# Optimization experiments

Hardware: AMD Instinct MI355X
Metric: run time of the kernel (lower is better)

Reference implementation:

```python
import jax, jax.numpy as jnp
import numpy as np

N = 100000      # nodes
E = 1600000     # edges (avg degree 16)
IN_C = 128
OUT_C = 64
HID = 2 * OUT_C  # 128


def setup_inputs() -> dict:
    key = jax.random.key(0)
    ks = jax.random.split(key, 8)
    x = jax.random.normal(ks[0], (N, IN_C), dtype=jnp.float32)
    edge_index = jax.random.randint(ks[1], (2, E), 0, N, dtype=jnp.int32)
    # Glorot-ish init for GCN weight matrices, zero bias (PyG default)
    w1 = jax.random.normal(ks[2], (IN_C, HID), dtype=jnp.float32) / np.sqrt(IN_C)
    b1 = jnp.zeros((HID,), jnp.float32)
    w_mu = jax.random.normal(ks[3], (HID, OUT_C), dtype=jnp.float32) / np.sqrt(HID)
    b_mu = jnp.zeros((OUT_C,), jnp.float32)
    w_ls = jax.random.normal(ks[4], (HID, OUT_C), dtype=jnp.float32) / np.sqrt(HID)
    b_ls = jnp.zeros((OUT_C,), jnp.float32)
    return {"x": x, "edge_index": edge_index, "w1": w1, "b1": b1,
            "w_mu": w_mu, "b_mu": b_mu, "w_ls": w_ls, "b_ls": b_ls}


def _gcn_conv(h, w, b, src, dst, norm, n):
    # linear transform, then normalized sparse aggregation src -> dst
    h = h @ w                                   # [N, out]
    msg = h[src] * norm[:, None]                # [E+N, out] gather
    out = jax.ops.segment_sum(msg, dst, num_segments=n)  # scatter-add
    return out + b


def reference(x, edge_index, w1, b1, w_mu, b_mu, w_ls, b_ls):
    n = x.shape[0]
    # GCN normalization with self-loops (edge_weight=None -> all ones)
    loops = jnp.arange(n, dtype=edge_index.dtype)
    src = jnp.concatenate([edge_index[0], loops])
    dst = jnp.concatenate([edge_index[1], loops])
    ew = jnp.ones(src.shape[0], dtype=x.dtype)
    deg = jax.ops.segment_sum(ew, dst, num_segments=n)
    dinv = jnp.where(deg > 0, jax.lax.rsqrt(jnp.maximum(deg, 1e-12)), 0.0)
    norm = dinv[src] * ew * dinv[dst]           # D^-1/2 A_hat D^-1/2

    h = jax.nn.relu(_gcn_conv(x, w1, b1, src, dst, norm, n))
    mu = _gcn_conv(h, w_mu, b_mu, src, dst, norm, n)
    logstd = _gcn_conv(h, w_ls, b_ls, src, dst, norm, n)
    return (mu, logstd)
```

## Files before the change

### kernel.cpp

```cpp
#include <hip/hip_runtime.h>
#include <hip/hip_bf16.h>

#define CH 128
#define OC 64
#define NBINS 1024
#define NCHK  256
#define BSH   7

typedef __attribute__((ext_vector_type(4))) float f32x4;
typedef __attribute__((ext_vector_type(8))) float f32x8;
typedef __attribute__((ext_vector_type(8))) short bf16x8;
typedef __attribute__((ext_vector_type(8))) ushort u16x8;

static __device__ __forceinline__ float bf2f(ushort u) {
  return __uint_as_float(((unsigned)u) << 16);
}
static __device__ __forceinline__ ushort f2bf(float f) {
  __hip_bfloat16 h = __float2bfloat16(f);
  return *reinterpret_cast<ushort*>(&h);
}
static __device__ __forceinline__ void fma8(float w, u16x8 v, f32x8& a) {
#pragma unroll
  for (int j = 0; j < 8; j++) a[j] = fmaf(w, bf2f((ushort)v[j]), a[j]);
}

__global__ void k_tobf(const float* __restrict__ x, ushort* __restrict__ y, int n) {
  int i = (blockIdx.x * blockDim.x + threadIdx.x) * 4;
  if (i < n) {
    float4 v = *(const float4*)&x[i];
    ushort4 o; o.x = f2bf(v.x); o.y = f2bf(v.y); o.z = f2bf(v.z); o.w = f2bf(v.w);
    *(ushort4*)&y[i] = o;
  }
}

__global__ void k_prep(const float* __restrict__ w1, const float* __restrict__ wmu,
                       const float* __restrict__ wls, const float* __restrict__ bmu,
                       const float* __restrict__ bls, ushort* __restrict__ Wt0,
                       ushort* __restrict__ Wt1, float* __restrict__ bc) {
  int idx = blockIdx.x * 256 + threadIdx.x;
  int c = idx >> 7, k = idx & 127;
  Wt0[c * 128 + k] = f2bf(w1[k * 128 + c]);
  float v = (c < 64) ? wmu[k * 64 + c] : wls[k * 64 + (c - 64)];
  Wt1[c * 128 + k] = f2bf(v);
  if (idx < 128) bc[idx] = (idx < 64) ? bmu[idx] : bls[idx - 64];
}


__global__ __launch_bounds__(256) void k_s1(const int* __restrict__ dst,
                                            int* __restrict__ bcnt, int ne, int cs) {
  __shared__ int h[NBINS];
  for (int j = threadIdx.x; j < NBINS; j += 256) h[j] = 0;
  __syncthreads();
  int e0 = blockIdx.x * cs, e1 = min(e0 + cs, ne);
  for (int e = e0 + threadIdx.x; e < e1; e += 256)
    atomicAdd(&h[dst[e] >> BSH], 1);
  __syncthreads();
  for (int j = threadIdx.x; j < NBINS; j += 256)
    bcnt[blockIdx.x * NBINS + j] = h[j];
}

__global__ __launch_bounds__(256) void k_s2a(const int* __restrict__ bcnt,
                                             int* __restrict__ curT,
                                             int* __restrict__ total) {
  __shared__ int s[NCHK];
  int b = blockIdx.x, t = threadIdx.x;
  int v = bcnt[t * NBINS + b];
  s[t] = v; __syncthreads();
  for (int off = 1; off < NCHK; off <<= 1) {
    int u = (t >= off) ? s[t - off] : 0;
    __syncthreads();
    s[t] += u;
    __syncthreads();
  }
  curT[b * NCHK + t] = s[t] - v;
  if (t == NCHK - 1) total[b] = s[t];
}

__global__ void k_s2b(const int* __restrict__ total, int* __restrict__ base) {
  __shared__ int s[256];
  int t = threadIdx.x;
  int loc[4]; int sum = 0;
#pragma unroll
  for (int j = 0; j < 4; j++) { loc[j] = total[t * 4 + j]; sum += loc[j]; }
  s[t] = sum; __syncthreads();
  int own = sum;
  for (int off = 1; off < 256; off <<= 1) {
    int u = (t >= off) ? s[t - off] : 0;
    __syncthreads();
    s[t] += u;
    __syncthreads();
  }
  int excl = s[t] - own;
#pragma unroll
  for (int j = 0; j < 4; j++) { base[t * 4 + j] = excl; excl += loc[j]; }
  if (t == 255) base[NBINS] = excl;
}

__global__ __launch_bounds__(256) void k_s3(const int* __restrict__ src,
    const int* __restrict__ dst, const int* __restrict__ curT,
    const int* __restrict__ base, int2* __restrict__ rec, int ne, int cs) {
  __shared__ int lcur[NBINS];
  int blk = blockIdx.x;
  for (int b = threadIdx.x; b < NBINS; b += 256)
    lcur[b] = curT[b * NCHK + blk] + base[b];
  __syncthreads();
  int e0 = blk * cs, e1 = min(e0 + cs, ne);
  for (int e = e0 + threadIdx.x; e < e1; e += 256) {
    int d = dst[e], sv = src[e];
    int pos = atomicAdd(&lcur[d >> BSH], 1);
    rec[pos] = make_int2(sv, d);
  }
}

__global__ __launch_bounds__(256) void k_s4(const int2* __restrict__ rec,
    const int* __restrict__ base, int* __restrict__ deg, int nn) {
  __shared__ int h[128];
  int b = blockIdx.x;
  if (threadIdx.x < 128) h[threadIdx.x] = 0;
  __syncthreads();
  int r0 = base[b], r1 = base[b + 1];
  for (int r = r0 + threadIdx.x; r < r1; r += 256)
    atomicAdd(&h[rec[r].y & 127], 1);
  __syncthreads();
  if (threadIdx.x < 128) {
    int node = (b << BSH) + threadIdx.x;
    if (node < nn) deg[node] = h[threadIdx.x];
  }
}

__global__ __launch_bounds__(256) void k_s5(const int2* __restrict__ rec,
    const int* __restrict__ base, const int* __restrict__ rowptr,
    const int* __restrict__ deg, unsigned* __restrict__ csr, int nn) {
  __shared__ int lcur[128];
  int b = blockIdx.x;
  if (threadIdx.x < 128) {
    int node = (b << BSH) + threadIdx.x;
    lcur[threadIdx.x] = (node < nn) ? rowptr[node] : 0;
  }
  __syncthreads();
  int r0 = base[b], r1 = base[b + 1];
  for (int r = r0 + threadIdx.x; r < r1; r += 256) {
    int2 rc = rec[r];
    int pos = atomicAdd(&lcur[rc.y & 127], 1);
    unsigned ds = (unsigned)min(deg[rc.x], 32767);
    csr[pos] = (unsigned)rc.x | (ds << 17);
  }
}


__global__ void k_scan1(const int* __restrict__ deg, int* __restrict__ bsum, int n) {
  __shared__ int s[256];
  int tid = threadIdx.x;
  int base = blockIdx.x * 2048;
  int sum = 0;
#pragma unroll
  for (int j = 0; j < 8; j++) {
    int idx = base + tid * 8 + j;
    if (idx < n) sum += deg[idx];
  }
  s[tid] = sum; __syncthreads();
  for (int off = 128; off > 0; off >>= 1) {
    if (tid < off) s[tid] += s[tid + off];
    __syncthreads();
  }
  if (tid == 0) bsum[blockIdx.x] = s[0];
}

__global__ void k_scan2(int* bsum, int nb) {
  __shared__ int s[256];
  int tid = threadIdx.x;
  int v = (tid < nb) ? bsum[tid] : 0;
  s[tid] = v; __syncthreads();
  for (int off = 1; off < 256; off <<= 1) {
    int t = (tid >= off) ? s[tid - off] : 0;
    __syncthreads();
    s[tid] += t;
    __syncthreads();
  }
  if (tid < nb) bsum[tid] = s[tid] - v;
}

__global__ void k_scan3(const int* __restrict__ deg, const int* __restrict__ bsum,
                        int* __restrict__ rowptr, float* __restrict__ dinv, int n) {
  __shared__ int s[256];
  int tid = threadIdx.x;
  int base = blockIdx.x * 2048;
  int local[8]; int sum = 0;
#pragma unroll
  for (int j = 0; j < 8; j++) {
    int idx = base + tid * 8 + j;
    int d = (idx < n) ? deg[idx] : 0;
    local[j] = d; sum += d;
  }
  s[tid] = sum; __syncthreads();
  int own = sum;
  for (int off = 1; off < 256; off <<= 1) {
    int t = (tid >= off) ? s[tid - off] : 0;
    __syncthreads();
    s[tid] += t;
    __syncthreads();
  }
  int excl = s[tid] - own + bsum[blockIdx.x];
#pragma unroll
  for (int j = 0; j < 8; j++) {
    int idx = base + tid * 8 + j;
    if (idx < n) {
      rowptr[idx] = excl;
      excl += local[j];
      dinv[idx] = rsqrtf((float)(local[j] + 1));
    }
  }
}

template<int MODE>
__global__ __launch_bounds__(256) void k_agg(const ushort* __restrict__ in,
                      ushort* __restrict__ o16, float* __restrict__ oA,
                      float* __restrict__ oB, const float* __restrict__ bc,
                      const int* __restrict__ rowptr, const int* __restrict__ deg,
                      const unsigned* __restrict__ csr, const float* __restrict__ dinv,
                      int n) {
  int i = blockIdx.x * 16 + (threadIdx.x >> 4);
  if (i >= n) return;
  int lane = threadIdx.x & 15;
  size_t loff = (size_t)lane * 8;
  int beg = rowptr[i];
  int cnt = deg[i];
  float di = dinv[i];
  u16x8 xv = *(const u16x8*)&in[(size_t)i * CH + loff];
  f32x8 acc = {0.f, 0.f, 0.f, 0.f, 0.f, 0.f, 0.f, 0.f};

  unsigned rec[8]; u16x8 row[4];
#pragma unroll
  for (int j = 0; j < 8; j++) rec[j] = (j < cnt) ? csr[beg + j] : 0u;
#pragma unroll
  for (int j = 0; j < 4; j++)
    if (j < cnt) row[j] = *(const u16x8*)&in[(size_t)(rec[j] & 0x1FFFFu) * CH + loff];

  int k = 0;
  while (cnt - k > 4) {
    unsigned nrec[4]; u16x8 nrow[4];
#pragma unroll
    for (int j = 0; j < 4; j++)
      nrec[j] = (k + 8 + j < cnt) ? csr[beg + k + 8 + j] : 0u;
#pragma unroll
    for (int j = 0; j < 4; j++)
      nrow[j] = (k + 4 + j < cnt)
              ? *(const u16x8*)&in[(size_t)(rec[4 + j] & 0x1FFFFu) * CH + loff]
              : row[j];
#pragma unroll
    for (int j = 0; j < 4; j++) {
      float w = rsqrtf((float)((rec[j] >> 17) + 1u));
      fma8(w, row[j], acc);
    }
#pragma unroll
    for (int j = 0; j < 4; j++) { rec[j] = rec[4 + j]; rec[4 + j] = nrec[j]; row[j] = nrow[j]; }
    k += 4;
  }
#pragma unroll
  for (int j = 0; j < 4; j++) {
    if (k + j < cnt) {
      float w = rsqrtf((float)((rec[j] >> 17) + 1u));
      fma8(w, row[j], acc);
    }
  }
  fma8(di, xv, acc);
  if (MODE == 0) {
    u16x8 o;
#pragma unroll
    for (int j = 0; j < 8; j++) o[j] = (short)f2bf(acc[j] * di);
    *(u16x8*)&o16[(size_t)i * CH + loff] = o;
  } else {
    f32x8 b8 = *(const f32x8*)&bc[lane * 8];
    f32x8 o;
#pragma unroll
    for (int j = 0; j < 8; j++) o[j] = acc[j] * di + b8[j];
    if (lane < 8) *(f32x8*)&oA[(size_t)i * OC + lane * 8] = o;
    else          *(f32x8*)&oB[(size_t)i * OC + (lane - 8) * 8] = o;
  }
}

__global__ __launch_bounds__(256) void k_fused(const ushort* __restrict__ A,
    const ushort* __restrict__ Wt0, const float* __restrict__ b1,
    const ushort* __restrict__ Wt1, ushort* __restrict__ P, int ntiles) {
  __shared__ ushort hs[16][136];
  int colg = threadIdx.x >> 6;
  int lane = threadIdx.x & 63;
  int l15 = lane & 15;
  int lk = (lane >> 4) * 8;
  bf16x8 bfrag1[2][4], bfrag2[2][4];
  float bias1[2];
#pragma unroll
  for (int ct = 0; ct < 2; ct++) {
    int bcol = colg * 32 + ct * 16 + l15;
#pragma unroll
    for (int kt = 0; kt < 4; kt++) {
      bfrag1[ct][kt] = *(const bf16x8*)&Wt0[(size_t)bcol * 128 + kt * 32 + lk];
      bfrag2[ct][kt] = *(const bf16x8*)&Wt1[(size_t)bcol * 128 + kt * 32 + lk];
    }
    bias1[ct] = b1[bcol];
  }
  for (int t = blockIdx.x; t < ntiles; t += gridDim.x) {
    const ushort* ap = &A[(size_t)(t * 16 + l15) * CH + lk];
    bf16x8 af[4];
#pragma unroll
    for (int kt = 0; kt < 4; kt++) af[kt] = *(const bf16x8*)&ap[kt * 32];
    f32x4 acc1[2] = {{0.f, 0.f, 0.f, 0.f}, {0.f, 0.f, 0.f, 0.f}};
#pragma unroll
    for (int ct = 0; ct < 2; ct++)
#pragma unroll
      for (int kt = 0; kt < 4; kt++)
        acc1[ct] = __builtin_amdgcn_mfma_f32_16x16x32_bf16(af[kt], bfrag1[ct][kt], acc1[ct], 0, 0, 0);
#pragma unroll
    for (int ct = 0; ct < 2; ct++) {
      int col = colg * 32 + ct * 16 + l15;
#pragma unroll
      for (int r = 0; r < 4; r++)
        hs[(lane >> 4) * 4 + r][col] = f2bf(fmaxf(acc1[ct][r] + bias1[ct], 0.f));
    }
    __syncthreads();
    bf16x8 af2[4];
#pragma unroll
    for (int kt = 0; kt < 4; kt++) af2[kt] = *(const bf16x8*)&hs[l15][kt * 32 + lk];
    f32x4 acc2[2] = {{0.f, 0.f, 0.f, 0.f}, {0.f, 0.f, 0.f, 0.f}};
#pragma unroll
    for (int ct = 0; ct < 2; ct++)
#pragma unroll
      for (int kt = 0; kt < 4; kt++)
        acc2[ct] = __builtin_amdgcn_mfma_f32_16x16x32_bf16(af2[kt], bfrag2[ct][kt], acc2[ct], 0, 0, 0);
#pragma unroll
    for (int ct = 0; ct < 2; ct++) {
      int col = colg * 32 + ct * 16 + l15;
#pragma unroll
      for (int r = 0; r < 4; r++) {
        int node = t * 16 + (lane >> 4) * 4 + r;
        P[(size_t)node * CH + col] = f2bf(acc2[ct][r]);
      }
    }
    __syncthreads();
  }
}


extern "C" void kernel_launch(void* const* d_in, const int* in_sizes, int n_in,
                              void* d_out, int out_size, void* d_ws, size_t ws_size,
                              hipStream_t stream) {
  const float* x   = (const float*)d_in[0];
  const int*   ei  = (const int*)d_in[1];
  const float* w1  = (const float*)d_in[2];
  const float* b1  = (const float*)d_in[3];
  const float* wmu = (const float*)d_in[4];
  const float* bmu = (const float*)d_in[5];
  const float* wls = (const float*)d_in[6];
  const float* bls = (const float*)d_in[7];
  float* out = (float*)d_out;

  const int nn = in_sizes[0] / CH;
  const int ne = in_sizes[1] / 2;
  const int* srcp = ei;
  const int* dstp = ei + ne;

  ushort*   B0   = (ushort*)d_ws;
  ushort*   B1   = B0 + (size_t)nn * CH;
  unsigned* csr  = (unsigned*)(B1 + (size_t)nn * CH);
  int*      deg  = (int*)(csr + ne);
  int*      rowptr = deg + nn;
  float*    dinv = (float*)(rowptr + nn);
  int*      bsum = (int*)(dinv + nn);
  ushort*   Wt0  = (ushort*)(bsum + 256);
  ushort*   Wt1  = Wt0 + 128 * 128;
  float*    bc   = (float*)(Wt1 + 128 * 128);

  int2*     rec  = (int2*)B1;
  int*      bcnt = (int*)(rec + ne);
  int*      curT = bcnt + NCHK * NBINS;
  int*      btot = curT + NBINS * NCHK;
  int*      bbase= btot + NBINS;

  const int NBUK = (nn + 127) >> BSH;
  const int cs = (ne + NCHK - 1) / NCHK;
  const int NB = (nn + 2047) / 2048;

  k_s1 <<<NCHK, 256, 0, stream>>>(dstp, bcnt, ne, cs);
  k_s2a<<<NBINS, NCHK, 0, stream>>>(bcnt, curT, btot);
  k_s2b<<<1, 256, 0, stream>>>(btot, bbase);
  k_s3 <<<NCHK, 256, 0, stream>>>(srcp, dstp, curT, bbase, rec, ne, cs);
  k_s4 <<<NBUK, 256, 0, stream>>>(rec, bbase, deg, nn);
  k_scan1<<<NB, 256, 0, stream>>>(deg, bsum, nn);
  k_scan2<<<1, 256, 0, stream>>>(bsum, NB);
  k_scan3<<<NB, 256, 0, stream>>>(deg, bsum, rowptr, dinv, nn);
  k_s5 <<<NBUK, 256, 0, stream>>>(rec, bbase, rowptr, deg, csr, nn);

  k_tobf<<<((nn * CH / 4) + 255) / 256, 256, 0, stream>>>(x, B0, nn * CH);
  k_prep<<<64, 256, 0, stream>>>(w1, wmu, wls, bmu, bls, Wt0, Wt1, bc);

  const int AB = (nn + 15) / 16;
  const int ntiles = nn / 16;

  k_agg<0><<<AB, 256, 0, stream>>>(B0, B1, nullptr, nullptr, nullptr,
                                   rowptr, deg, csr, dinv, nn);
  k_fused<<<1024, 256, 0, stream>>>(B1, Wt0, b1, Wt1, B0, ntiles);
  k_agg<1><<<AB, 256, 0, stream>>>(B0, nullptr, out, out + (size_t)nn * OC, bc,
                                   rowptr, deg, csr, dinv, nn);
}
```

Before: 228.1 us.

## Fuse first aggregation with MLP GEMMs, pack edge records, merge scans and prep kernels

Several independent changes are bundled. Edge records are packed into one 32-bit word (source<<7 | local dst) to halve scatter traffic. The per-bucket histogram now computes rowptr and dinv directly with a local scan, replacing three global scan kernels. The bf16 conversion and weight prep are merged into one launch. The first aggregation is fused into the MFMA two-layer transform kernel, which removes the intermediate aggregated buffer round-trip. The fused kernel runs the gather per tile inside a persistent grid, which may reduce latency hiding compared with a full one-block-per-16-nodes grid, and it drops the trailing barrier between tiles.

After: 227.4 us. No clear change (-0.3%).

```diff
diff --git a/kernel.cpp b/kernel.cpp
--- a/kernel.cpp
+++ b/kernel.cpp
@@ -24,25 +24,25 @@
   for (int j = 0; j < 8; j++) a[j] = fmaf(w, bf2f((ushort)v[j]), a[j]);
 }
 
-__global__ void k_tobf(const float* __restrict__ x, ushort* __restrict__ y, int n) {
-  int i = (blockIdx.x * blockDim.x + threadIdx.x) * 4;
-  if (i < n) {
+__global__ void k_pre(const float* __restrict__ x, ushort* __restrict__ y, int nx,
+                      const float* __restrict__ w1, const float* __restrict__ wmu,
+                      const float* __restrict__ wls, const float* __restrict__ bmu,
+                      const float* __restrict__ bls, ushort* __restrict__ Wt0,
+                      ushort* __restrict__ Wt1, float* __restrict__ bc) {
+  int gid = blockIdx.x * 256 + threadIdx.x;
+  int i = gid * 4;
+  if (i < nx) {
     float4 v = *(const float4*)&x[i];
     ushort4 o; o.x = f2bf(v.x); o.y = f2bf(v.y); o.z = f2bf(v.z); o.w = f2bf(v.w);
     *(ushort4*)&y[i] = o;
   }
-}
-
-__global__ void k_prep(const float* __restrict__ w1, const float* __restrict__ wmu,
-                       const float* __restrict__ wls, const float* __restrict__ bmu,
-                       const float* __restrict__ bls, ushort* __restrict__ Wt0,
-                       ushort* __restrict__ Wt1, float* __restrict__ bc) {
-  int idx = blockIdx.x * 256 + threadIdx.x;
-  int c = idx >> 7, k = idx & 127;
-  Wt0[c * 128 + k] = f2bf(w1[k * 128 + c]);
-  float v = (c < 64) ? wmu[k * 64 + c] : wls[k * 64 + (c - 64)];
-  Wt1[c * 128 + k] = f2bf(v);
-  if (idx < 128) bc[idx] = (idx < 64) ? bmu[idx] : bls[idx - 64];
+  if (gid < 16384) {
+    int c = gid >> 7, k = gid & 127;
+    Wt0[c * 128 + k] = f2bf(w1[k * 128 + c]);
+    float v = (c < 64) ? wmu[k * 64 + c] : wls[k * 64 + (c - 64)];
+    Wt1[c * 128 + k] = f2bf(v);
+    if (gid < 128) bc[gid] = (gid < 64) ? bmu[gid] : bls[gid - 64];
+  }
 }
 
 
@@ -98,7 +98,7 @@
 
 __global__ __launch_bounds__(256) void k_s3(const int* __restrict__ src,
     const int* __restrict__ dst, const int* __restrict__ curT,
-    const int* __restrict__ base, int2* __restrict__ rec, int ne, int cs) {
+    const int* __restrict__ base, unsigned* __restrict__ rec, int ne, int cs) {
   __shared__ int lcur[NBINS];
   int blk = blockIdx.x;
   for (int b = threadIdx.x; b < NBINS; b += 256)
@@ -108,236 +108,201 @@
   for (int e = e0 + threadIdx.x; e < e1; e += 256) {
     int d = dst[e], sv = src[e];
     int pos = atomicAdd(&lcur[d >> BSH], 1);
-    rec[pos] = make_int2(sv, d);
-  }
-}
-
-__global__ __launch_bounds__(256) void k_s4(const int2* __restrict__ rec,
-    const int* __restrict__ base, int* __restrict__ deg, int nn) {
+    rec[pos] = ((unsigned)sv << BSH) | (unsigned)(d & 127);
+  }
+}
+
+__global__ __launch_bounds__(256) void k_s4a(const unsigned* __restrict__ rec,
+    const int* __restrict__ base, int* __restrict__ deg, int* __restrict__ rowptr,
+    float* __restrict__ dinv, int nn) {
   __shared__ int h[128];
-  int b = blockIdx.x;
-  if (threadIdx.x < 128) h[threadIdx.x] = 0;
+  __shared__ int sc[128];
+  int b = blockIdx.x, tid = threadIdx.x;
+  if (tid < 128) h[tid] = 0;
   __syncthreads();
   int r0 = base[b], r1 = base[b + 1];
-  for (int r = r0 + threadIdx.x; r < r1; r += 256)
-    atomicAdd(&h[rec[r].y & 127], 1);
-  __syncthreads();
-  if (threadIdx.x < 128) {
-    int node = (b << BSH) + threadIdx.x;
-    if (node < nn) deg[node] = h[threadIdx.x];
-  }
-}
-
-__global__ __launch_bounds__(256) void k_s5(const int2* __restrict__ rec,
+  for (int r = r0 + tid; r < r1; r += 256)
+    atomicAdd(&h[rec[r] & 127], 1);
+  __syncthreads();
+  if (tid < 128) sc[tid] = h[tid];
+  __syncthreads();
+  for (int off = 1; off < 128; off <<= 1) {
+    int v = 0;
+    if (tid < 128 && tid >= off) v = sc[tid - off];
+    __syncthreads();
+    if (tid < 128) sc[tid] += v;
+    __syncthreads();
+  }
+  if (tid < 128) {
+    int node = (b << BSH) + tid;
+    if (node < nn) {
+      int d = h[tid];
+      deg[node] = d;
+      rowptr[node] = r0 + sc[tid] - d;
+      dinv[node] = rsqrtf((float)(d + 1));
+    }
+  }
+}
+
+__global__ __launch_bounds__(256) void k_s5(const unsigned* __restrict__ rec,
     const int* __restrict__ base, const int* __restrict__ rowptr,
     const int* __restrict__ deg, unsigned* __restrict__ csr, int nn) {
   __shared__ int lcur[128];
-  int b = blockIdx.x;
-  if (threadIdx.x < 128) {
-    int node = (b << BSH) + threadIdx.x;
-    lcur[threadIdx.x] = (node < nn) ? rowptr[node] : 0;
+  int b = blockIdx.x, tid = threadIdx.x;
+  if (tid < 128) {
+    int node = (b << BSH) + tid;
+    lcur[tid] = (node < nn) ? rowptr[node] : 0;
   }
   __syncthreads();
   int r0 = base[b], r1 = base[b + 1];
-  for (int r = r0 + threadIdx.x; r < r1; r += 256) {
-    int2 rc = rec[r];
-    int pos = atomicAdd(&lcur[rc.y & 127], 1);
-    unsigned ds = (unsigned)min(deg[rc.x], 32767);
-    csr[pos] = (unsigned)rc.x | (ds << 17);
-  }
-}
-
-
-__global__ void k_scan1(const int* __restrict__ deg, int* __restrict__ bsum, int n) {
-  __shared__ int s[256];
+  for (int r = r0 + tid; r < r1; r += 256) {
+    unsigned rc = rec[r];
+    int s = (int)(rc >> BSH);
+    int pos = atomicAdd(&lcur[rc & 127], 1);
+    unsigned ds = (unsigned)min(deg[s], 32767);
+    csr[pos] = (unsigned)s | (ds << 17);
+  }
+}
+
+static __device__ __forceinline__ f32x8 gather_core(const ushort* __restrict__ in,
+    const int* __restrict__ rowptr, const int* __restrict__ deg,
+    const unsigned* __restrict__ csr, const float* __restrict__ dinv,
+    int i, int lane16, float& di_out) {
+  size_t loff = (size_t)lane16 * 8;
+  int beg = rowptr[i];
+  int cnt = deg[i];
+  float di = dinv[i];
+  u16x8 xv = *(const u16x8*)&in[(size_t)i * CH + loff];
+  f32x8 acc = {0.f, 0.f, 0.f, 0.f, 0.f, 0.f, 0.f, 0.f};
+
+  unsigned rec[8]; u16x8 row[4];
+#pragma unroll
+  for (int j = 0; j < 8; j++) rec[j] = (j < cnt) ? csr[beg + j] : 0u;
+#pragma unroll
+  for (int j = 0; j < 4; j++)
+    if (j < cnt) row[j] = *(const u16x8*)&in[(size_t)(rec[j] & 0x1FFFFu) * CH + loff];
+
+  int k = 0;
+  while (cnt - k > 4) {
+    unsigned nrec[4]; u16x8 nrow[4];
+#pragma unroll
+    for (int j = 0; j < 4; j++)
+      nrec[j] = (k + 8 + j < cnt) ? csr[beg + k + 8 + j] : 0u;
+#pragma unroll
+    for (int j = 0; j < 4; j++)
+      nrow[j] = (k + 4 + j < cnt)
+              ? *(const u16x8*)&in[(size_t)(rec[4 + j] & 0x1FFFFu) * CH + loff]
+              : row[j];
+#pragma unroll
+    for (int j = 0; j < 4; j++) {
+      float w = rsqrtf((float)((rec[j] >> 17) + 1u));
+      fma8(w, row[j], acc);
+    }
+#pragma unroll
+    for (int j = 0; j < 4; j++) { rec[j] = rec[4 + j]; rec[4 + j] = nrec[j]; row[j] = nrow[j]; }
+    k += 4;
+  }
+#pragma unroll
+  for (int j = 0; j < 4; j++) {
+    if (k + j < cnt) {
+      float w = rsqrtf((float)((rec[j] >> 17) + 1u));
+      fma8(w, row[j], acc);
+    }
+  }
+  fma8(di, xv, acc);
+  di_out = di;
+  return acc;
+}
+
+__global__ __launch_bounds__(256) void k_aggemm(const ushort* __restrict__ in,
+    const int* __restrict__ rowptr, const int* __restrict__ deg,
+    const unsigned* __restrict__ csr, const float* __restrict__ dinv,
+    const ushort* __restrict__ Wt0, const float* __restrict__ b1,
+    const ushort* __restrict__ Wt1, ushort* __restrict__ P, int ntiles) {
+  __shared__ ushort as_[16][136];
+  __shared__ ushort hs[16][136];
   int tid = threadIdx.x;
-  int base = blockIdx.x * 2048;
-  int sum = 0;
-#pragma unroll
-  for (int j = 0; j < 8; j++) {
-    int idx = base + tid * 8 + j;
-    if (idx < n) sum += deg[idx];
-  }
-  s[tid] = sum; __syncthreads();
-  for (int off = 128; off > 0; off >>= 1) {
-    if (tid < off) s[tid] += s[tid + off];
-    __syncthreads();
-  }
-  if (tid == 0) bsum[blockIdx.x] = s[0];
-}
-
-__global__ void k_scan2(int* bsum, int nb) {
-  __shared__ int s[256];
-  int tid = threadIdx.x;
-  int v = (tid < nb) ? bsum[tid] : 0;
-  s[tid] = v; __syncthreads();
-  for (int off = 1; off < 256; off <<= 1) {
-    int t = (tid >= off) ? s[tid - off] : 0;
-    __syncthreads();
-    s[tid] += t;
-    __syncthreads();
-  }
-  if (tid < nb) bsum[tid] = s[tid] - v;
-}
-
-__global__ void k_scan3(const int* __restrict__ deg, const int* __restrict__ bsum,
-                        int* __restrict__ rowptr, float* __restrict__ dinv, int n) {
-  __shared__ int s[256];
-  int tid = threadIdx.x;
-  int base = blockIdx.x * 2048;
-  int local[8]; int sum = 0;
-#pragma unroll
-  for (int j = 0; j < 8; j++) {
-    int idx = base + tid * 8 + j;
-    int d = (idx < n) ? deg[idx] : 0;
-    local[j] = d; sum += d;
-  }
-  s[tid] = sum; __syncthreads();
-  int own = sum;
-  for (int off = 1; off < 256; off <<= 1) {
-    int t = (tid >= off) ? s[tid - off] : 0;
-    __syncthreads();
-    s[tid] += t;
-    __syncthreads();
-  }
-  int excl = s[tid] - own + bsum[blockIdx.x];
-#pragma unroll
-  for (int j = 0; j < 8; j++) {
-    int idx = base + tid * 8 + j;
-    if (idx < n) {
-      rowptr[idx] = excl;
-      excl += local[j];
-      dinv[idx] = rsqrtf((float)(local[j] + 1));
-    }
-  }
-}
-
-template<int MODE>
-__global__ __launch_bounds__(256) void k_agg(const ushort* __restrict__ in,
-                      ushort* __restrict__ o16, float* __restrict__ oA,
-                      float* __restrict__ oB, const float* __restrict__ bc,
+  int node16 = tid >> 4, lane16 = tid & 15;
+  int wv = tid >> 6;
+  int lane = tid & 63;
+  int l15 = lane & 15;
+  int lk = (lane >> 4) * 8;
+  bf16x8 bfrag1[2][4], bfrag2[2][4];
+  float bias1[2];
+#pragma unroll
+  for (int ct = 0; ct < 2; ct++) {
+    int bcol = wv * 32 + ct * 16 + l15;
+#pragma unroll
+    for (int kt = 0; kt < 4; kt++) {
+      bfrag1[ct][kt] = *(const bf16x8*)&Wt0[(size_t)bcol * 128 + kt * 32 + lk];
+      bfrag2[ct][kt] = *(const bf16x8*)&Wt1[(size_t)bcol * 128 + kt * 32 + lk];
+    }
+    bias1[ct] = b1[bcol];
+  }
+  for (int t = blockIdx.x; t < ntiles; t += gridDim.x) {
+    int i = t * 16 + node16;
+    float di;
+    f32x8 acc = gather_core(in, rowptr, deg, csr, dinv, i, lane16, di);
+    u16x8 o;
+#pragma unroll
+    for (int j = 0; j < 8; j++) o[j] = (short)f2bf(acc[j] * di);
+    *(u16x8*)&as_[node16][lane16 * 8] = o;
+    __syncthreads();
+    bf16x8 af[4];
+#pragma unroll
+    for (int kt = 0; kt < 4; kt++) af[kt] = *(const bf16x8*)&as_[l15][kt * 32 + lk];
+    f32x4 a1[2] = {{0.f, 0.f, 0.f, 0.f}, {0.f, 0.f, 0.f, 0.f}};
+#pragma unroll
+    for (int ct = 0; ct < 2; ct++)
+#pragma unroll
+      for (int kt = 0; kt < 4; kt++)
+        a1[ct] = __builtin_amdgcn_mfma_f32_16x16x32_bf16(af[kt], bfrag1[ct][kt], a1[ct], 0, 0, 0);
+#pragma unroll
+    for (int ct = 0; ct < 2; ct++) {
+      int col = wv * 32 + ct * 16 + l15;
+#pragma unroll
+      for (int r = 0; r < 4; r++)
+        hs[(lane >> 4) * 4 + r][col] = f2bf(fmaxf(a1[ct][r] + bias1[ct], 0.f));
+    }
+    __syncthreads();
+    bf16x8 af2[4];
+#pragma unroll
+    for (int kt = 0; kt < 4; kt++) af2[kt] = *(const bf16x8*)&hs[l15][kt * 32 + lk];
+    f32x4 a2[2] = {{0.f, 0.f, 0.f, 0.f}, {0.f, 0.f, 0.f, 0.f}};
+#pragma unroll
+    for (int ct = 0; ct < 2; ct++)
+#pragma unroll
+      for (int kt = 0; kt < 4; kt++)
+        a2[ct] = __builtin_amdgcn_mfma_f32_16x16x32_bf16(af2[kt], bfrag2[ct][kt], a2[ct], 0, 0, 0);
+#pragma unroll
+    for (int ct = 0; ct < 2; ct++) {
+      int col = wv * 32 + ct * 16 + l15;
+#pragma unroll
+      for (int r = 0; r < 4; r++) {
+        int node = t * 16 + (lane >> 4) * 4 + r;
+        P[(size_t)node * CH + col] = f2bf(a2[ct][r]);
+      }
+    }
+  }
+}
+
+__global__ __launch_bounds__(256) void k_aggout(const ushort* __restrict__ in,
+                      float* __restrict__ oA, float* __restrict__ oB,
+                      const float* __restrict__ bc,
                       const int* __restrict__ rowptr, const int* __restrict__ deg,
                       const unsigned* __restrict__ csr, const float* __restrict__ dinv,
                       int n) {
   int i = blockIdx.x * 16 + (threadIdx.x >> 4);
   if (i >= n) return;
   int lane = threadIdx.x & 15;
-  size_t loff = (size_t)lane * 8;
-  int beg = rowptr[i];
-  int cnt = deg[i];
-  float di = dinv[i];
-  u16x8 xv = *(const u16x8*)&in[(size_t)i * CH + loff];
-  f32x8 acc = {0.f, 0.f, 0.f, 0.f, 0.f, 0.f, 0.f, 0.f};
-
-  unsigned rec[8]; u16x8 row[4];
-#pragma unroll
-  for (int j = 0; j < 8; j++) rec[j] = (j < cnt) ? csr[beg + j] : 0u;
-#pragma unroll
-  for (int j = 0; j < 4; j++)
-    if (j < cnt) row[j] = *(const u16x8*)&in[(size_t)(rec[j] & 0x1FFFFu) * CH + loff];
-
-  int k = 0;
-  while (cnt - k > 4) {
-    unsigned nrec[4]; u16x8 nrow[4];
-#pragma unroll
-    for (int j = 0; j < 4; j++)
-      nrec[j] = (k + 8 + j < cnt) ? csr[beg + k + 8 + j] : 0u;
-#pragma unroll
-    for (int j = 0; j < 4; j++)
-      nrow[j] = (k + 4 + j < cnt)
-              ? *(const u16x8*)&in[(size_t)(rec[4 + j] & 0x1FFFFu) * CH + loff]
-              : row[j];
-#pragma unroll
-    for (int j = 0; j < 4; j++) {
-      float w = rsqrtf((float)((rec[j] >> 17) + 1u));
-      fma8(w, row[j], acc);
-    }
-#pragma unroll
-    for (int j = 0; j < 4; j++) { rec[j] = rec[4 + j]; rec[4 + j] = nrec[j]; row[j] = nrow[j]; }
-    k += 4;
-  }
-#pragma unroll
-  for (int j = 0; j < 4; j++) {
-    if (k + j < cnt) {
-      float w = rsqrtf((float)((rec[j] >> 17) + 1u));
-      fma8(w, row[j], acc);
-    }
-  }
-  fma8(di, xv, acc);
-  if (MODE == 0) {
-    u16x8 o;
-#pragma unroll
-    for (int j = 0; j < 8; j++) o[j] = (short)f2bf(acc[j] * di);
-    *(u16x8*)&o16[(size_t)i * CH + loff] = o;
-  } else {
-    f32x8 b8 = *(const f32x8*)&bc[lane * 8];
-    f32x8 o;
-#pragma unroll
-    for (int j = 0; j < 8; j++) o[j] = acc[j] * di + b8[j];
-    if (lane < 8) *(f32x8*)&oA[(size_t)i * OC + lane * 8] = o;
-    else          *(f32x8*)&oB[(size_t)i * OC + (lane - 8) * 8] = o;
-  }
-}
-
-__global__ __launch_bounds__(256) void k_fused(const ushort* __restrict__ A,
-    const ushort* __restrict__ Wt0, const float* __restrict__ b1,
-    const ushort* __restrict__ Wt1, ushort* __restrict__ P, int ntiles) {
-  __shared__ ushort hs[16][136];
-  int colg = threadIdx.x >> 6;
-  int lane = threadIdx.x & 63;
-  int l15 = lane & 15;
-  int lk = (lane >> 4) * 8;
-  bf16x8 bfrag1[2][4], bfrag2[2][4];
-  float bias1[2];
-#pragma unroll
-  for (int ct = 0; ct < 2; ct++) {
-    int bcol = colg * 32 + ct * 16 + l15;
-#pragma unroll
-    for (int kt = 0; kt < 4; kt++) {
-      bfrag1[ct][kt] = *(const bf16x8*)&Wt0[(size_t)bcol * 128 + kt * 32 + lk];
-      bfrag2[ct][kt] = *(const bf16x8*)&Wt1[(size_t)bcol * 128 + kt * 32 + lk];
-    }
-    bias1[ct] = b1[bcol];
-  }
-  for (int t = blockIdx.x; t < ntiles; t += gridDim.x) {
-    const ushort* ap = &A[(size_t)(t * 16 + l15) * CH + lk];
-    bf16x8 af[4];
-#pragma unroll
-    for (int kt = 0; kt < 4; kt++) af[kt] = *(const bf16x8*)&ap[kt * 32];
-    f32x4 acc1[2] = {{0.f, 0.f, 0.f, 0.f}, {0.f, 0.f, 0.f, 0.f}};
-#pragma unroll
-    for (int ct = 0; ct < 2; ct++)
-#pragma unroll
-      for (int kt = 0; kt < 4; kt++)
-        acc1[ct] = __builtin_amdgcn_mfma_f32_16x16x32_bf16(af[kt], bfrag1[ct][kt], acc1[ct], 0, 0, 0);
-#pragma unroll
-    for (int ct = 0; ct < 2; ct++) {
-      int col = colg * 32 + ct * 16 + l15;
-#pragma unroll
-      for (int r = 0; r < 4; r++)
-        hs[(lane >> 4) * 4 + r][col] = f2bf(fmaxf(acc1[ct][r] + bias1[ct], 0.f));
-    }
-    __syncthreads();
-    bf16x8 af2[4];
-#pragma unroll
-    for (int kt = 0; kt < 4; kt++) af2[kt] = *(const bf16x8*)&hs[l15][kt * 32 + lk];
-    f32x4 acc2[2] = {{0.f, 0.f, 0.f, 0.f}, {0.f, 0.f, 0.f, 0.f}};
-#pragma unroll
-    for (int ct = 0; ct < 2; ct++)
-#pragma unroll
-      for (int kt = 0; kt < 4; kt++)
-        acc2[ct] = __builtin_amdgcn_mfma_f32_16x16x32_bf16(af2[kt], bfrag2[ct][kt], acc2[ct], 0, 0, 0);
-#pragma unroll
-    for (int ct = 0; ct < 2; ct++) {
-      int col = colg * 32 + ct * 16 + l15;
-#pragma unroll
-      for (int r = 0; r < 4; r++) {
-        int node = t * 16 + (lane >> 4) * 4 + r;
-        P[(size_t)node * CH + col] = f2bf(acc2[ct][r]);
-      }
-    }
-    __syncthreads();
-  }
+  float di;
+  f32x8 acc = gather_core(in, rowptr, deg, csr, dinv, i, lane, di);
+  f32x8 b8 = *(const f32x8*)&bc[lane * 8];
+  f32x8 o;
+#pragma unroll
+  for (int j = 0; j < 8; j++) o[j] = acc[j] * di + b8[j];
+  if (lane < 8) *(f32x8*)&oA[(size_t)i * OC + lane * 8] = o;
+  else          *(f32x8*)&oB[(size_t)i * OC + (lane - 8) * 8] = o;
 }
 
 
@@ -365,12 +330,11 @@
   int*      deg  = (int*)(csr + ne);
   int*      rowptr = deg + nn;
   float*    dinv = (float*)(rowptr + nn);
-  int*      bsum = (int*)(dinv + nn);
-  ushort*   Wt0  = (ushort*)(bsum + 256);
+  ushort*   Wt0  = (ushort*)(dinv + nn);
   ushort*   Wt1  = Wt0 + 128 * 128;
   float*    bc   = (float*)(Wt1 + 128 * 128);
 
-  int2*     rec  = (int2*)B1;
+  unsigned* rec  = (unsigned*)B1;
   int*      bcnt = (int*)(rec + ne);
   int*      curT = bcnt + NCHK * NBINS;
   int*      btot = curT + NBINS * NCHK;
@@ -378,27 +342,19 @@
 
   const int NBUK = (nn + 127) >> BSH;
   const int cs = (ne + NCHK - 1) / NCHK;
-  const int NB = (nn + 2047) / 2048;
 
   k_s1 <<<NCHK, 256, 0, stream>>>(dstp, bcnt, ne, cs);
   k_s2a<<<NBINS, NCHK, 0, stream>>>(bcnt, curT, btot);
   k_s2b<<<1, 256, 0, stream>>>(btot, bbase);
   k_s3 <<<NCHK, 256, 0, stream>>>(srcp, dstp, curT, bbase, rec, ne, cs);
-  k_s4 <<<NBUK, 256, 0, stream>>>(rec, bbase, deg, nn);
-  k_scan1<<<NB, 256, 0, stream>>>(deg, bsum, nn);
-  k_scan2<<<1, 256, 0, stream>>>(bsum, NB);
-  k_scan3<<<NB, 256, 0, stream>>>(deg, bsum, rowptr, dinv, nn);
+  k_s4a<<<NBUK, 256, 0, stream>>>(rec, bbase, deg, rowptr, dinv, nn);
   k_s5 <<<NBUK, 256, 0, stream>>>(rec, bbase, rowptr, deg, csr, nn);
-
-  k_tobf<<<((nn * CH / 4) + 255) / 256, 256, 0, stream>>>(x, B0, nn * CH);
-  k_prep<<<64, 256, 0, stream>>>(w1, wmu, wls, bmu, bls, Wt0, Wt1, bc);
-
-  const int AB = (nn + 15) / 16;
+  k_pre<<<((nn * CH / 4) + 255) / 256, 256, 0, stream>>>(x, B0, nn * CH,
+                                 w1, wmu, wls, bmu, bls, Wt0, Wt1, bc);
+
   const int ntiles = nn / 16;
-
-  k_agg<0><<<AB, 256, 0, stream>>>(B0, B1, nullptr, nullptr, nullptr,
-                                   rowptr, deg, csr, dinv, nn);
-  k_fused<<<1024, 256, 0, stream>>>(B1, Wt0, b1, Wt1, B0, ntiles);
-  k_agg<1><<<AB, 256, 0, stream>>>(B0, nullptr, out, out + (size_t)nn * OC, bc,
-                                   rowptr, deg, csr, dinv, nn);
-}
+  k_aggemm<<<2048, 256, 0, stream>>>(B0, rowptr, deg, csr, dinv,
+                                     Wt0, b1, Wt1, B1, ntiles);
+  k_aggout<<<(nn + 15) / 16, 256, 0, stream>>>(B1, out, out + (size_t)nn * OC, bc,
+                                               rowptr, deg, csr, dinv, nn);
+}
```
